# Optimization experiments

Hardware: AMD Instinct MI355X
Metric: run time of the kernel (lower is better)

Reference implementation:

```python
import jax, jax.numpy as jnp
import numpy as np
import math

B, S, HID = 2, 2048, 1024
NH, HD = 16, 64
MAX_SEQ = 65536  # RoPE base from RotaryEmbedding


def _rope_tables(seq_len, dim):
    inv_freq = 1.0 / (MAX_SEQ ** (jnp.arange(0, dim, 2, dtype=jnp.float32) / dim))
    t = jnp.arange(seq_len, dtype=jnp.float32)
    freqs = jnp.einsum('i,j->ij', t, inv_freq)          # [S, dim/2]
    emb = jnp.concatenate([freqs, freqs], axis=-1)      # [S, dim]
    return jnp.cos(emb), jnp.sin(emb)


def _rotate_half(x):
    x1, x2 = jnp.split(x, 2, axis=-1)
    return jnp.concatenate([-x2, x1], axis=-1)


def setup_inputs() -> dict:
    key = jax.random.key(0)
    ks = jax.random.split(key, 9)
    std_qkv = 1.0 / math.sqrt(NH * HD)
    std_o = 1.0 / math.sqrt(HID)
    return {
        'input_embeds': jax.random.normal(ks[0], (B, S, HID), dtype=jnp.float32),
        'Wq': jax.random.normal(ks[1], (NH * HD, HID), dtype=jnp.float32) * std_qkv,
        'bq': jnp.zeros((NH * HD,), dtype=jnp.float32),
        'Wk': jax.random.normal(ks[2], (NH * HD, HID), dtype=jnp.float32) * std_qkv,
        'bk': jnp.zeros((NH * HD,), dtype=jnp.float32),
        'Wv': jax.random.normal(ks[3], (NH * HD, HID), dtype=jnp.float32) * std_qkv,
        'bv': jnp.zeros((NH * HD,), dtype=jnp.float32),
        'Wo': jax.random.normal(ks[4], (HID, NH * HD), dtype=jnp.float32) * std_o,
        'bo': jnp.zeros((HID,), dtype=jnp.float32),
    }


def reference(input_embeds, Wq, bq, Wk, bk, Wv, bv, Wo, bo):
    x = input_embeds
    b, s, _ = x.shape
    # QKV projections (torch Linear: x @ W.T + b)
    q = x @ Wq.T + bq
    k = x @ Wk.T + bk
    v = x @ Wv.T + bv
    # [B, S, NH*HD] -> [B, NH, S, HD]
    q = q.reshape(b, s, NH, HD).transpose(0, 2, 1, 3)
    k = k.reshape(b, s, NH, HD).transpose(0, 2, 1, 3)
    v = v.reshape(b, s, NH, HD).transpose(0, 2, 1, 3)
    # RoPE
    cos, sin = _rope_tables(s, HD)  # [S, HD]
    q = q * cos + _rotate_half(q) * sin
    k = k * cos + _rotate_half(k) * sin
    # SDPA (non-causal, no mask)
    scale = 1.0 / math.sqrt(HD)
    scores = jnp.einsum('bhqd,bhkd->bhqk', q, k) * scale
    attn = jax.nn.softmax(scores, axis=-1)
    out = jnp.einsum('bhqk,bhkd->bhqd', attn, v)
    # [B, NH, S, HD] -> [B, S, NH*HD]
    out = out.transpose(0, 2, 1, 3).reshape(b, s, NH * HD)
    return out @ Wo.T + bo
```

## Files before the change

kernel.cpp:

```cpp
#include <hip/hip_runtime.h>
#include <cstdint>
#include <cstddef>

#define S_LEN 2048
#define NHEAD 16
#define HDIM  64
#define HID_  1024

typedef short s8v  __attribute__((ext_vector_type(8)));
typedef short s4v  __attribute__((ext_vector_type(4)));
typedef float f4v  __attribute__((ext_vector_type(4)));
typedef float f16v __attribute__((ext_vector_type(16)));

__device__ __forceinline__ short f2b(float x) {
    union { float f; unsigned u; } a; a.f = x;
    unsigned r = a.u + 0x7fffu + ((a.u >> 16) & 1u);
    return (short)(r >> 16);
}
__device__ __forceinline__ float b2f(short x) {
    union { unsigned u; float f; } a; a.u = ((unsigned)(unsigned short)x) << 16;
    return a.f;
}

__device__ __forceinline__ void gload_lds16(const void* g, void* l) {
    __builtin_amdgcn_global_load_lds(
        (__attribute__((address_space(1))) void*)const_cast<void*>(g),
        (__attribute__((address_space(3))) void*)l, 16, 0, 0);
}

__device__ __forceinline__ unsigned cvtpk(float a, float b) {
    unsigned r;
    asm("v_cvt_pk_bf16_f32 %0, %1, %2" : "=v"(r) : "v"(a), "v"(b));
    return r;
}
__device__ __forceinline__ void plswap(unsigned& a, unsigned& b) {
    asm("v_permlane32_swap_b32 %0, %1" : "+v"(a), "+v"(b));
}

__global__ __launch_bounds__(256) void f2b_kernel(const float* __restrict__ in,
                                                  short* __restrict__ out, int n4) {
    int i = blockIdx.x * 256 + threadIdx.x;
    if (i >= n4) return;
    float4 v = reinterpret_cast<const float4*>(in)[i];
    s4v o;
    o[0] = f2b(v.x); o[1] = f2b(v.y); o[2] = f2b(v.z); o[3] = f2b(v.w);
    reinterpret_cast<s4v*>(out)[i] = o;
}

__global__ __launch_bounds__(256) void f2bw_kernel(
    const float* __restrict__ Wq, const float* __restrict__ Wk,
    const float* __restrict__ Wv, const float* __restrict__ Wo,
    short* __restrict__ Wcat, short* __restrict__ Wob)
{
    const int y = blockIdx.y;
    const float* src = (y == 0) ? Wq : (y == 1) ? Wk : (y == 2) ? Wv : Wo;
    short* dst = (y < 3) ? (Wcat + (size_t)y * 1048576) : Wob;
    int i = blockIdx.x * 256 + threadIdx.x;
    float4 v = reinterpret_cast<const float4*>(src)[i];
    s4v o;
    o[0] = f2b(v.x); o[1] = f2b(v.y); o[2] = f2b(v.z); o[3] = f2b(v.w);
    reinterpret_cast<s4v*>(dst)[i] = o;
}

__global__ __launch_bounds__(256) void rope_table_kernel(float2* __restrict__ tab) {
    int idx = blockIdx.x * 256 + threadIdx.x;
    int s = idx >> 5, j = idx & 31;
    float inv = exp2f(-0.5f * (float)j);
    float ang = (float)s * inv;
    float2 cs; cs.x = cosf(ang); cs.y = sinf(ang);
    tab[idx] = cs;
}

__global__ __launch_bounds__(256) void gemm_qkv(
    const short* __restrict__ A, const short* __restrict__ Bw,
    const float* __restrict__ bq, const float* __restrict__ bk,
    const float* __restrict__ bv,
    short* __restrict__ Qo, short* __restrict__ Ko, short* __restrict__ Vo,
    const float2* __restrict__ rtab)
{
    __shared__ short Asl[2][128 * 32];
    __shared__ short Bsl[2][128 * 32];
    const int t = threadIdx.x;
    const int lane = t & 63;
    const int l15 = lane & 15, l4 = lane >> 4;
    const int wid = t >> 6;
    const int blk = blockIdx.x;
    const int x = blk & 7, j = blk >> 3;
    const int tn = (x * 3 + j % 3) * 128;
    const int tm = (j / 3) * 128;
    const int K = 1024;
    const int wrow = (wid >> 1) * 64, wcol = (wid & 1) * 64;

    f4v acc[4][4];
#pragma unroll
    for (int i = 0; i < 4; ++i)
#pragma unroll
        for (int jj = 0; jj < 4; ++jj) acc[i][jj] = (f4v){0.f, 0.f, 0.f, 0.f};

    const int r0 = t >> 2;
    const int c0 = (t & 3) * 8;
    const int wbase = (t & ~63) * 8;

#define QSTAGE(buf, kt) do { const int k0_ = (kt) << 5;                            \
        gload_lds16(A  + (size_t)(tm + r0)      * K + k0_ + c0, &Asl[buf][wbase]);        \
        gload_lds16(A  + (size_t)(tm + 64 + r0) * K + k0_ + c0, &Asl[buf][2048 + wbase]); \
        gload_lds16(Bw + (size_t)(tn + r0)      * K + k0_ + c0, &Bsl[buf][wbase]);        \
        gload_lds16(Bw + (size_t)(tn + 64 + r0) * K + k0_ + c0, &Bsl[buf][2048 + wbase]); \
    } while (0)

    QSTAGE(0, 0);
    __syncthreads();
    int cur = 0;
    for (int kt = 0; kt < 32; ++kt) {
        if (kt < 31) QSTAGE(cur ^ 1, kt + 1);
        s8v af[4], bf[4];
#pragma unroll
        for (int i = 0; i < 4; ++i) {
            af[i] = *(const s8v*)&Asl[cur][(wrow + i * 16 + l15) * 32 + 8 * l4];
            bf[i] = *(const s8v*)&Bsl[cur][(wcol + i * 16 + l15) * 32 + 8 * l4];
        }
#pragma unroll
        for (int i = 0; i < 4; ++i)
#pragma unroll
            for (int jj = 0; jj < 4; ++jj)
                acc[i][jj] = __builtin_amdgcn_mfma_f32_16x16x32_bf16(af[i], bf[jj], acc[i][jj], 0, 0, 0);
        __syncthreads();
        cur ^= 1;
    }
#undef QSTAGE

    const int mode = tn >> 10;
    const float* bias = (mode == 0) ? bq : (mode == 1) ? bk : bv;
    short* outb = (mode == 0) ? Qo : (mode == 1) ? Ko : Vo;

    if (mode == 2) {
#pragma unroll
        for (int i = 0; i < 4; ++i) {
            int rowb = tm + wrow + i * 16 + l4 * 4;
            int b_ = rowb >> 11, s0 = rowb & 2047;
#pragma unroll
            for (int jj = 0; jj < 4; ++jj) {
                int col = tn + wcol + jj * 16 + l15;
                int cm = col & 1023;
                float bvv = bias[cm];
                int h = cm >> 6, d = col & 63;
                s4v o4;
#pragma unroll
                for (int r = 0; r < 4; ++r) o4[r] = f2b(acc[i][jj][r] + bvv);
                *(s4v*)&outb[((size_t)((b_ * NHEAD + h) * 64 + d)) * S_LEN + s0] = o4;
            }
        }
    } else {
        int h = ((tn & 1023) + wcol) >> 6;
        const float osc = (mode == 0) ? 0.180336880111f : 1.0f;
#pragma unroll
        for (int i = 0; i < 4; ++i) {
#pragma unroll
            for (int r = 0; r < 4; ++r) {
                int row = tm + wrow + i * 16 + l4 * 4 + r;
                int b_ = row >> 11, s = row & 2047;
                float2 cs0 = rtab[(s << 5) + l15];
                float2 cs1 = rtab[(s << 5) + 16 + l15];
#pragma unroll
                for (int jj = 0; jj < 4; ++jj) {
                    int col = tn + wcol + jj * 16 + l15;
                    int cm = col & 1023;
                    int d = col & 63;
                    float v  = acc[i][jj][r]     + bias[cm];
                    float vp = acc[i][jj ^ 2][r] + bias[cm ^ 32];
                    float2 cs = (jj & 1) ? cs1 : cs0;
                    float res = (d < 32) ? (v * cs.x - vp * cs.y)
                                         : (v * cs.x + vp * cs.y);
                    outb[(((size_t)(b_ * NHEAD + h) * S_LEN + s) << 6) + d] = f2b(res * osc);
                }
            }
        }
    }
}

__global__ __launch_bounds__(256) void gemm_o(
    const short* __restrict__ A, const short* __restrict__ Bw,
    const float* __restrict__ bias, float* __restrict__ outf)
{
    __shared__ short Asl[2][64 * 32];
    __shared__ short Bsl[2][128 * 32];
    const int t = threadIdx.x;
    const int lane = t & 63;
    const int l15 = lane & 15, l4 = lane >> 4;
    const int wid = t >> 6;
    const int blk = blockIdx.x;
    const int tn = (blk & 7) * 128;
    const int tm = (blk >> 3) * 64;
    const int K = 1024, N = 1024;
    const int wrow = (wid >> 1) * 32, wcol = (wid & 1) * 64;

    f4v acc[2][4];
#pragma unroll
    for (int i = 0; i < 2; ++i)
#pragma unroll
        for (int jj = 0; jj < 4; ++jj) acc[i][jj] = (f4v){0.f, 0.f, 0.f, 0.f};

    const int r0 = t >> 2;
    const int c0 = (t & 3) * 8;
    const int wbase = (t & ~63) * 8;

#define OSTAGE(buf, kt) do { const int k0_ = (kt) << 5;                            \
        gload_lds16(A  + (size_t)(tm + r0)      * K + k0_ + c0, &Asl[buf][wbase]);        \
        gload_lds16(Bw + (size_t)(tn + r0)      * K + k0_ + c0, &Bsl[buf][wbase]);        \
        gload_lds16(Bw + (size_t)(tn + 64 + r0) * K + k0_ + c0, &Bsl[buf][2048 + wbase]); \
    } while (0)

    OSTAGE(0, 0);
    __syncthreads();
    int cur = 0;
    for (int kt = 0; kt < 32; ++kt) {
        if (kt < 31) OSTAGE(cur ^ 1, kt + 1);
        s8v af[2], bf[4];
#pragma unroll
        for (int i = 0; i < 2; ++i)
            af[i] = *(const s8v*)&Asl[cur][(wrow + i * 16 + l15) * 32 + 8 * l4];
#pragma unroll
        for (int jj = 0; jj < 4; ++jj)
            bf[jj] = *(const s8v*)&Bsl[cur][(wcol + jj * 16 + l15) * 32 + 8 * l4];
#pragma unroll
        for (int i = 0; i < 2; ++i)
#pragma unroll
            for (int jj = 0; jj < 4; ++jj)
                acc[i][jj] = __builtin_amdgcn_mfma_f32_16x16x32_bf16(af[i], bf[jj], acc[i][jj], 0, 0, 0);
        __syncthreads();
        cur ^= 1;
    }
#undef OSTAGE

#pragma unroll
    for (int i = 0; i < 2; ++i) {
        int rowb = tm + wrow + i * 16 + l4 * 4;
#pragma unroll
        for (int jj = 0; jj < 4; ++jj) {
            int col = tn + wcol + jj * 16 + l15;
            float bv = bias[col];
#pragma unroll
            for (int r = 0; r < 4; ++r)
                outf[(size_t)(rowb + r) * N + col] = acc[i][jj][r] + bv;
        }
    }
}

#define SWB(row, bofs) ((bofs) ^ (((row) & 7) << 4))

__global__ __launch_bounds__(256, 4) void attn_split(
    const short* __restrict__ Q, const short* __restrict__ K,
    const short* __restrict__ Vt,
    short* __restrict__ P0, short* __restrict__ P1, float2* __restrict__ ML)
{
    __shared__ short Kl[4096];
    __shared__ short Vl[4096];

    const int t = threadIdx.x, lane = t & 63;
    const int wid = t >> 6;
    const int q5 = lane & 31, hi = lane >> 5;

    const int blk = blockIdx.x;
    const int x = blk & 7, j = blk >> 3;
    const int bh = x * 4 + (j & 3);
    const int rest = j >> 2;
    const int qb = rest & 15, split = rest >> 4;
    const int kt0 = split * 16;

    const short* Qb = Q + (size_t)bh * S_LEN * 64;
    const char*  Kb = (const char*)(K  + (size_t)bh * S_LEN * 64);
    const char*  Vb = (const char*)(Vt + (size_t)bh * S_LEN * 64);
    const int qrow = qb * 128 + wid * 32 + q5;

    s8v qf[4];
#pragma unroll
    for (int sl = 0; sl < 4; ++sl)
        qf[sl] = *(const s8v*)&Qb[(size_t)qrow * 64 + sl * 16 + hi * 8];

    f16v oacc[2];
#pragma unroll
    for (int dt = 0; dt < 2; ++dt)
#pragma unroll
        for (int e = 0; e < 16; ++e) oacc[dt][e] = 0.f;
    float m2 = -1e30f, lsum = 0.f;

    const int skey  = t >> 3;
    const int sboff = (t & 7) * 16;
    const int sw    = SWB(skey, sboff);
    const size_t kgoff = (size_t)skey * 128  + sboff;
    const size_t vgoff = (size_t)skey * 4096 + sboff;
    char* KlB = (char*)Kl;
    char* VlB = (char*)Vl;
    const int w0 = skey * 128 + sw;
    const int w1 = w0 + 32 * 128;

    {
        const size_t kbB = (size_t)kt0 * 64 * 128;
        const size_t vbB = (size_t)kt0 * 64 * 2;
        s8v g0 = *(const s8v*)(Kb + kbB + kgoff);
        s8v g1 = *(const s8v*)(Kb + kbB + kgoff + 32 * 128);
        s8v g2 = *(const s8v*)(Vb + vbB + vgoff);
        s8v g3 = *(const s8v*)(Vb + vbB + vgoff + 32 * 4096);
        *(s8v*)(KlB + w0) = g0; *(s8v*)(KlB + w1) = g1;
        *(s8v*)(VlB + w0) = g2; *(s8v*)(VlB + w1) = g3;
    }
    __syncthreads();

    for (int kt = kt0; kt < kt0 + 16; ++kt) {
        s8v g0, g1, g2, g3;
        const bool pre = (kt < kt0 + 15);
        if (pre) {
            const size_t kbB = (size_t)(kt + 1) * 64 * 128;
            const size_t vbB = (size_t)(kt + 1) * 64 * 2;
            g0 = *(const s8v*)(Kb + kbB + kgoff);
            g1 = *(const s8v*)(Kb + kbB + kgoff + 32 * 128);
            g2 = *(const s8v*)(Vb + vbB + vgoff);
            g3 = *(const s8v*)(Vb + vbB + vgoff + 32 * 4096);
        }

        f16v sc[2];
#pragma unroll
        for (int c = 0; c < 2; ++c) {
#pragma unroll
            for (int e = 0; e < 16; ++e) sc[c][e] = 0.f;
            const int krow = c * 32 + q5;
            const char* kbase = KlB + krow * 128;
            __builtin_amdgcn_s_setprio(1);
#pragma unroll
            for (int sl = 0; sl < 4; ++sl) {
                s8v kf = *(const s8v*)(kbase + SWB(krow, sl * 32 + hi * 16));
                sc[c] = __builtin_amdgcn_mfma_f32_32x32x16_bf16(kf, qf[sl], sc[c], 0, 0, 0);
            }
            __builtin_amdgcn_s_setprio(0);
        }

        float m8[8];
#pragma unroll
        for (int e = 0; e < 8; ++e)
            m8[e] = fmaxf(fmaxf(sc[0][e], sc[0][e + 8]), fmaxf(sc[1][e], sc[1][e + 8]));
        float pm = fmaxf(fmaxf(fmaxf(m8[0], m8[4]), fmaxf(m8[1], m8[5])),
                         fmaxf(fmaxf(m8[2], m8[6]), fmaxf(m8[3], m8[7])));
        pm = fmaxf(pm, __shfl_xor(pm, 32, 64));
        if (__any(pm > m2 + 8.0f)) {
            float m2n = fmaxf(m2, pm);
            float fr = __builtin_amdgcn_exp2f(m2 - m2n);
            lsum *= fr;
#pragma unroll
            for (int dt = 0; dt < 2; ++dt)
#pragma unroll
                for (int e = 0; e < 16; ++e) oacc[dt][e] *= fr;
            m2 = m2n;
        }
#pragma unroll
        for (int c = 0; c < 2; ++c)
#pragma unroll
            for (int e = 0; e < 16; ++e)
                sc[c][e] = __builtin_amdgcn_exp2f(sc[c][e] - m2);
        float sum8[8];
#pragma unroll
        for (int e = 0; e < 8; ++e)
            sum8[e] = (sc[0][e] + sc[0][e + 8]) + (sc[1][e] + sc[1][e + 8]);
        lsum += ((sum8[0] + sum8[4]) + (sum8[1] + sum8[5])) +
                ((sum8[2] + sum8[6]) + (sum8[3] + sum8[7]));

#pragma unroll
        for (int c = 0; c < 2; ++c) {
#pragma unroll
            for (int ks = 0; ks < 2; ++ks) {
                const int b0 = ks * 8;
                unsigned x0 = cvtpk(sc[c][b0 + 0], sc[c][b0 + 1]);
                unsigned y0 = cvtpk(sc[c][b0 + 4], sc[c][b0 + 5]);
                unsigned x1 = cvtpk(sc[c][b0 + 2], sc[c][b0 + 3]);
                unsigned y1 = cvtpk(sc[c][b0 + 6], sc[c][b0 + 7]);
                plswap(x0, y0);
                plswap(x1, y1);
                union { unsigned u[4]; s8v s; } pf;
                pf.u[0] = x0; pf.u[1] = x1; pf.u[2] = y0; pf.u[3] = y1;
                __builtin_amdgcn_s_setprio(1);
#pragma unroll
                for (int dt = 0; dt < 2; ++dt) {
                    const int vrow = dt * 32 + q5;
                    s8v vf = *(const s8v*)(VlB + vrow * 128 +
                                           SWB(vrow, c * 64 + ks * 32 + hi * 16));
                    oacc[dt] = __builtin_amdgcn_mfma_f32_32x32x16_bf16(vf, pf.s, oacc[dt], 0, 0, 0);
                }
                __builtin_amdgcn_s_setprio(0);
            }
        }

        __syncthreads();
        if (pre) {
            *(s8v*)(KlB + w0) = g0; *(s8v*)(KlB + w1) = g1;
            *(s8v*)(VlB + w0) = g2; *(s8v*)(VlB + w1) = g3;
        }
        __syncthreads();
    }

    float ls = lsum + __shfl_xor(lsum, 32, 64);
    float inv = 1.0f / ls;
    short* Pp = (split ? P1 : P0) + ((size_t)bh * S_LEN + qrow) * 64;
#pragma unroll
    for (int dt = 0; dt < 2; ++dt)
#pragma unroll
        for (int g = 0; g < 4; ++g) {
            s4v o4;
#pragma unroll
            for (int jj = 0; jj < 4; ++jj) o4[jj] = f2b(oacc[dt][g * 4 + jj] * inv);
            const int d0 = dt * 32 + g * 8 + hi * 4;
            *(s4v*)&Pp[d0] = o4;
        }
    if (hi == 0) {
        float2 ml; ml.x = m2; ml.y = ls;
        ML[(size_t)split * (32 * S_LEN) + bh * S_LEN + qrow] = ml;
    }
}

__global__ __launch_bounds__(256) void attn_combine(
    const short* __restrict__ P0, const short* __restrict__ P1,
    const float2* __restrict__ ML, short* __restrict__ Obf)
{
    int idx = blockIdx.x * 256 + threadIdx.x;
    int row = idx >> 3;
    int d0 = (idx & 7) * 8;
    float2 a = ML[row];
    float2 b = ML[32 * S_LEN + row];
    float m = fmaxf(a.x, b.x);
    float w0 = a.y * exp2f(a.x - m);
    float w1 = b.y * exp2f(b.x - m);
    float inv = 1.0f / (w0 + w1);
    w0 *= inv; w1 *= inv;
    s8v v0 = *(const s8v*)&P0[(size_t)row * 64 + d0];
    s8v v1 = *(const s8v*)&P1[(size_t)row * 64 + d0];
    s8v o;
#pragma unroll
    for (int e = 0; e < 8; ++e) o[e] = f2b(w0 * b2f(v0[e]) + w1 * b2f(v1[e]));
    int bh = row >> 11, s = row & 2047;
    int b_ = bh >> 4, h = bh & 15;
    *(s8v*)&Obf[((size_t)(b_ * S_LEN + s)) * HID_ + h * 64 + d0] = o;
}

extern "C" void kernel_launch(void* const* d_in, const int* in_sizes, int n_in,
                              void* d_out, int out_size, void* d_ws, size_t ws_size,
                              hipStream_t stream)
{
    const float* X  = (const float*)d_in[0];
    const float* Wq = (const float*)d_in[1];
    const float* bq = (const float*)d_in[2];
    const float* Wk = (const float*)d_in[3];
    const float* bk = (const float*)d_in[4];
    const float* Wv = (const float*)d_in[5];
    const float* bv = (const float*)d_in[6];
    const float* Wo = (const float*)d_in[7];
    const float* bo = (const float*)d_in[8];
    float* out = (float*)d_out;

    char* ws = (char*)d_ws;
    short*  Xb   = (short*) (ws);
    short*  Wcat = (short*) (ws + ( 8u << 20));
    short*  Wob  = (short*) (ws + (14u << 20));
    float2* rtab = (float2*)(ws + (16u << 20));
    short*  Qbh  = (short*) (ws + (17u << 20));
    short*  Kbh  = (short*) (ws + (25u << 20));
    short*  Vbh  = (short*) (ws + (33u << 20));
    short*  Obf  = (short*) (ws + (41u << 20));
    short*  P0   = (short*) (ws);
    short*  P1   = (short*) d_out;
    float2* ML   = (float2*)((char*)d_out + (8u << 20));

    f2b_kernel<<<4096, 256, 0, stream>>>(X, Xb, 1048576);
    f2bw_kernel<<<dim3(1024, 4), 256, 0, stream>>>(Wq, Wk, Wv, Wo, Wcat, Wob);
    rope_table_kernel<<<256, 256, 0, stream>>>(rtab);

    gemm_qkv<<<768, 256, 0, stream>>>(Xb, Wcat, bq, bk, bv, Qbh, Kbh, Vbh, rtab);
    attn_split<<<1024, 256, 0, stream>>>(Qbh, Kbh, Vbh, P0, P1, ML);
    attn_combine<<<2048, 256, 0, stream>>>(P0, P1, ML, Obf);
    gemm_o<<<512, 256, 0, stream>>>(Obf, Wob, bo, out);
}
```

Before: 153.6 us.

## Merge prep kernels, use partial vmcnt waits in GEMMs, interleave QK MFMAs

Folds the three preprocessing launches (X cast, weight cast, RoPE table) into a single kernel to cut launch overhead. In both GEMMs, the full __syncthreads after each prefetch is replaced by an explicit s_waitcnt vmcnt(N) plus s_barrier, so the next stage's loads stay in flight while the current tile is consumed. In attention, the two K-chunk MFMA chains are interleaved to give independent MFMAs back-to-back. The manual waitcnt relies on the LDS-direct loads being tracked by vmcnt and on the count matching exactly; a wrong count would be a race.

```diff
diff --git a/kernel.cpp b/kernel.cpp
--- a/kernel.cpp
+++ b/kernel.cpp
@@ -37,38 +37,38 @@
     asm("v_permlane32_swap_b32 %0, %1" : "+v"(a), "+v"(b));
 }
 
-__global__ __launch_bounds__(256) void f2b_kernel(const float* __restrict__ in,
-                                                  short* __restrict__ out, int n4) {
-    int i = blockIdx.x * 256 + threadIdx.x;
-    if (i >= n4) return;
-    float4 v = reinterpret_cast<const float4*>(in)[i];
-    s4v o;
-    o[0] = f2b(v.x); o[1] = f2b(v.y); o[2] = f2b(v.z); o[3] = f2b(v.w);
-    reinterpret_cast<s4v*>(out)[i] = o;
-}
-
-__global__ __launch_bounds__(256) void f2bw_kernel(
+__global__ __launch_bounds__(256) void prep_kernel(
+    const float* __restrict__ X,
     const float* __restrict__ Wq, const float* __restrict__ Wk,
     const float* __restrict__ Wv, const float* __restrict__ Wo,
-    short* __restrict__ Wcat, short* __restrict__ Wob)
-{
-    const int y = blockIdx.y;
-    const float* src = (y == 0) ? Wq : (y == 1) ? Wk : (y == 2) ? Wv : Wo;
-    short* dst = (y < 3) ? (Wcat + (size_t)y * 1048576) : Wob;
-    int i = blockIdx.x * 256 + threadIdx.x;
-    float4 v = reinterpret_cast<const float4*>(src)[i];
-    s4v o;
-    o[0] = f2b(v.x); o[1] = f2b(v.y); o[2] = f2b(v.z); o[3] = f2b(v.w);
-    reinterpret_cast<s4v*>(dst)[i] = o;
-}
-
-__global__ __launch_bounds__(256) void rope_table_kernel(float2* __restrict__ tab) {
-    int idx = blockIdx.x * 256 + threadIdx.x;
-    int s = idx >> 5, j = idx & 31;
-    float inv = exp2f(-0.5f * (float)j);
-    float ang = (float)s * inv;
-    float2 cs; cs.x = cosf(ang); cs.y = sinf(ang);
-    tab[idx] = cs;
+    short* __restrict__ Xb, short* __restrict__ Wcat, short* __restrict__ Wob,
+    float2* __restrict__ rtab)
+{
+    const int bid = blockIdx.x;
+    if (bid < 8192) {
+        const float* src;
+        short* dst;
+        int i;
+        if (bid < 4096) {
+            src = X; dst = Xb; i = bid * 256 + threadIdx.x;
+        } else {
+            int w = (bid - 4096) >> 10;
+            src = (w == 0) ? Wq : (w == 1) ? Wk : (w == 2) ? Wv : Wo;
+            dst = (w < 3) ? (Wcat + (size_t)w * 1048576) : Wob;
+            i = ((bid - 4096) & 1023) * 256 + threadIdx.x;
+        }
+        float4 v = reinterpret_cast<const float4*>(src)[i];
+        s4v o;
+        o[0] = f2b(v.x); o[1] = f2b(v.y); o[2] = f2b(v.z); o[3] = f2b(v.w);
+        reinterpret_cast<s4v*>(dst)[i] = o;
+    } else {
+        int idx = (bid - 8192) * 256 + threadIdx.x;
+        int s = idx >> 5, j = idx & 31;
+        float inv = exp2f(-0.5f * (float)j);
+        float ang = (float)s * inv;
+        float2 cs; cs.x = cosf(ang); cs.y = sinf(ang);
+        rtab[idx] = cs;
+    }
 }
 
 __global__ __launch_bounds__(256) void gemm_qkv(
@@ -109,10 +109,16 @@
     } while (0)
 
     QSTAGE(0, 0);
-    __syncthreads();
     int cur = 0;
     for (int kt = 0; kt < 32; ++kt) {
-        if (kt < 31) QSTAGE(cur ^ 1, kt + 1);
+        if (kt < 31) {
+            QSTAGE(cur ^ 1, kt + 1);
+            asm volatile("s_waitcnt vmcnt(4)" ::: "memory");
+        } else {
+            asm volatile("s_waitcnt vmcnt(0)" ::: "memory");
+        }
+        __builtin_amdgcn_s_barrier();
+        __builtin_amdgcn_sched_barrier(0);
         s8v af[4], bf[4];
 #pragma unroll
         for (int i = 0; i < 4; ++i) {
@@ -124,7 +130,7 @@
 #pragma unroll
             for (int jj = 0; jj < 4; ++jj)
                 acc[i][jj] = __builtin_amdgcn_mfma_f32_16x16x32_bf16(af[i], bf[jj], acc[i][jj], 0, 0, 0);
-        __syncthreads();
+        __builtin_amdgcn_s_barrier();
         cur ^= 1;
     }
 #undef QSTAGE
@@ -211,10 +217,16 @@
     } while (0)
 
     OSTAGE(0, 0);
-    __syncthreads();
     int cur = 0;
     for (int kt = 0; kt < 32; ++kt) {
-        if (kt < 31) OSTAGE(cur ^ 1, kt + 1);
+        if (kt < 31) {
+            OSTAGE(cur ^ 1, kt + 1);
+            asm volatile("s_waitcnt vmcnt(3)" ::: "memory");
+        } else {
+            asm volatile("s_waitcnt vmcnt(0)" ::: "memory");
+        }
+        __builtin_amdgcn_s_barrier();
+        __builtin_amdgcn_sched_barrier(0);
         s8v af[2], bf[4];
 #pragma unroll
         for (int i = 0; i < 2; ++i)
@@ -227,7 +239,7 @@
 #pragma unroll
             for (int jj = 0; jj < 4; ++jj)
                 acc[i][jj] = __builtin_amdgcn_mfma_f32_16x16x32_bf16(af[i], bf[jj], acc[i][jj], 0, 0, 0);
-        __syncthreads();
+        __builtin_amdgcn_s_barrier();
         cur ^= 1;
     }
 #undef OSTAGE
@@ -320,16 +332,18 @@
 
         f16v sc[2];
 #pragma unroll
-        for (int c = 0; c < 2; ++c) {
-#pragma unroll
-            for (int e = 0; e < 16; ++e) sc[c][e] = 0.f;
-            const int krow = c * 32 + q5;
-            const char* kbase = KlB + krow * 128;
+        for (int e = 0; e < 16; ++e) { sc[0][e] = 0.f; sc[1][e] = 0.f; }
+        {
+            const int kr0 = q5, kr1 = 32 + q5;
+            const char* kb0 = KlB + kr0 * 128;
+            const char* kb1 = KlB + kr1 * 128;
             __builtin_amdgcn_s_setprio(1);
 #pragma unroll
             for (int sl = 0; sl < 4; ++sl) {
-                s8v kf = *(const s8v*)(kbase + SWB(krow, sl * 32 + hi * 16));
-                sc[c] = __builtin_amdgcn_mfma_f32_32x32x16_bf16(kf, qf[sl], sc[c], 0, 0, 0);
+                s8v kf0 = *(const s8v*)(kb0 + SWB(kr0, sl * 32 + hi * 16));
+                s8v kf1 = *(const s8v*)(kb1 + SWB(kr1, sl * 32 + hi * 16));
+                sc[0] = __builtin_amdgcn_mfma_f32_32x32x16_bf16(kf0, qf[sl], sc[0], 0, 0, 0);
+                sc[1] = __builtin_amdgcn_mfma_f32_32x32x16_bf16(kf1, qf[sl], sc[1], 0, 0, 0);
             }
             __builtin_amdgcn_s_setprio(0);
         }
@@ -467,10 +481,7 @@
     short*  P1   = (short*) d_out;
     float2* ML   = (float2*)((char*)d_out + (8u << 20));
 
-    f2b_kernel<<<4096, 256, 0, stream>>>(X, Xb, 1048576);
-    f2bw_kernel<<<dim3(1024, 4), 256, 0, stream>>>(Wq, Wk, Wv, Wo, Wcat, Wob);
-    rope_table_kernel<<<256, 256, 0, stream>>>(rtab);
-
+    prep_kernel<<<8448, 256, 0, stream>>>(X, Wq, Wk, Wv, Wo, Xb, Wcat, Wob, rtab);
     gemm_qkv<<<768, 256, 0, stream>>>(Xb, Wcat, bq, bk, bv, Qbh, Kbh, Vbh, rtab);
     attn_split<<<1024, 256, 0, stream>>>(Qbh, Kbh, Vbh, P0, P1, ML);
     attn_combine<<<2048, 256, 0, stream>>>(P0, P1, ML, Obf);
```

Result: no change. 151.3 us (-1.5%).
